# Performance work log

Measured on AMD Instinct MI355X. Metric: run time of the kernel, lower is better.

## Reference

```python
import math
import jax, jax.numpy as jnp
import numpy as np

B, L, D = 8, 512, 32
SEQ_LEN = 512.0
N_PATCHES, N_REF = 16, 32
LAT, HM = 128, 4
FH, NL, FF = 8, 3, 128
PRED = 96

def _time_embed(t, d):
    # interleaved sin/cos embedding, matching PositionalEmbedding's div_term
    div = jnp.exp(jnp.arange(0, d, 2, dtype=jnp.float32) * (-math.log(10000.0) / d))
    ang = t[..., None] * div
    out = jnp.zeros(t.shape + (d,), dtype=jnp.float32)
    return out.at[..., 0::2].set(jnp.sin(ang)).at[..., 1::2].set(jnp.cos(ang))

def _layernorm(x, g, b):
    mu = jnp.mean(x, axis=-1, keepdims=True)
    var = jnp.var(x, axis=-1, keepdims=True)
    return (x - mu) / jnp.sqrt(var + 1e-5) * g + b

def _mha(z, Wq, Wk, Wv, Wo, bq, bk, bv, bo):
    N, S, dm = z.shape
    hd = dm // FH
    q = (z @ Wq + bq).reshape(N, S, FH, hd)
    k = (z @ Wk + bk).reshape(N, S, FH, hd)
    v = (z @ Wv + bv).reshape(N, S, FH, hd)
    s = jnp.einsum('nqhe,nkhe->nhqk', q, k) / math.sqrt(hd)
    a = jax.nn.softmax(s, axis=-1)
    o = jnp.einsum('nhqk,nkhe->nqhe', a, v).reshape(N, S, dm)
    return o @ Wo + bo

def _forward(x, x_mark, x_mask, Wq, Wk, W_out, b_out, f_Wq, f_Wk, f_Wv, f_Wo, f_bq, f_bk, f_bv, f_bo, f_ln1_g, f_ln1_b, f_W1, f_b1, f_W2, f_b2, f_ln2_g, f_ln2_b, ln_f_g, ln_f_b, W_lin, b_lin):
    t = x_mark[:, :, 0]                                   # [B, L] irregular timestamps in [0, SEQ_LEN]
    edges = jnp.linspace(0.0, SEQ_LEN, N_PATCHES + 1)
    refs = jnp.linspace(0.0, SEQ_LEN, N_REF * N_PATCHES).reshape(N_PATCHES, N_REF)
    obs_valid = jnp.sum(x_mask, axis=-1) > 0              # [B, L]
    dk = LAT // HM
    Kmat = (_time_embed(t, LAT) @ Wk).reshape(B, L, HM, dk)
    v = x * x_mask                                        # mask values like `v = v * m` in original
    reprs = []
    for i in range(N_PATCHES):  # fixed small structural loop
        # _split_patch equivalent: per-channel masked attention is permutation
        # invariant, so the sort/scatter compaction reduces to masking.
        in_patch = (t >= edges[i]) & (t <= edges[i + 1]) & obs_valid   # [B, L]
        Qi = (_time_embed(refs[i], LAT) @ Wq).reshape(N_REF, HM, dk)
        scores = jnp.einsum('rhe,blhe->bhrl', Qi, Kmat) / math.sqrt(dk)
        cmask = x_mask * in_patch[..., None].astype(x.dtype)           # [B, L, D]
        neg = jnp.where(cmask[:, None, None, :, :] > 0, 0.0, -1e9)     # [B,1,1,L,D]
        p = jax.nn.softmax(scores[..., None] + neg, axis=3)            # [B,H,R,L,D]
        attn = jnp.einsum('bhrld,bld->brhd', p, v)                     # [B,R,H,D]
        reprs.append(attn.reshape(B, N_REF, HM * D) @ W_out + b_out)   # [B,R,D]
    rp = jnp.stack(reprs, axis=1)                          # [B, NP, R, D]
    z = rp.transpose(0, 3, 1, 2).reshape(B * D, N_PATCHES, N_REF)
    z = z + _time_embed(jnp.arange(N_PATCHES, dtype=jnp.float32), N_REF)[None]
    for l in range(NL):
        a = _mha(z, f_Wq[l], f_Wk[l], f_Wv[l], f_Wo[l], f_bq[l], f_bk[l], f_bv[l], f_bo[l])
        z = _layernorm(z + a, f_ln1_g[l], f_ln1_b[l])
        y = jax.nn.gelu(z @ f_W1[l] + f_b1[l]) @ f_W2[l] + f_b2[l]
        z = _layernorm(z + y, f_ln2_g[l], f_ln2_b[l])
    z = _layernorm(z, ln_f_g, ln_f_b)
    emb = z.reshape(B, D, N_PATCHES, N_REF).transpose(0, 1, 3, 2)      # [B, D, R, NP]
    out = emb.reshape(B, D, N_REF * N_PATCHES) @ W_lin + b_lin         # [B, D, PRED]
    return out.transpose(0, 2, 1)                          # [B, PRED, D]

def setup_inputs():
    key = jax.random.key(0)
    ks = jax.random.split(key, 30)
    def w(i, shape, fan_in):
        return jax.random.normal(ks[i], shape, jnp.float32) / math.sqrt(fan_in)
    return {
        'x': jax.random.normal(ks[0], (B, L, D), jnp.float32),
        'x_mark': jnp.sort(jax.random.uniform(ks[1], (B, L, 1), jnp.float32) * SEQ_LEN, axis=1),
        'x_mask': (jax.random.uniform(ks[2], (B, L, D), jnp.float32) < 0.8).astype(jnp.float32),
        'Wq': w(3, (LAT, LAT), LAT),
        'Wk': w(4, (LAT, LAT), LAT),
        'W_out': w(5, (HM * D, D), HM * D),
        'b_out': jnp.zeros((D,), jnp.float32),
        'f_Wq': w(6, (NL, N_REF, N_REF), N_REF),
        'f_Wk': w(7, (NL, N_REF, N_REF), N_REF),
        'f_Wv': w(8, (NL, N_REF, N_REF), N_REF),
        'f_Wo': w(9, (NL, N_REF, N_REF), N_REF),
        'f_bq': jnp.zeros((NL, N_REF), jnp.float32),
        'f_bk': jnp.zeros((NL, N_REF), jnp.float32),
        'f_bv': jnp.zeros((NL, N_REF), jnp.float32),
        'f_bo': jnp.zeros((NL, N_REF), jnp.float32),
        'f_ln1_g': jnp.ones((NL, N_REF), jnp.float32),
        'f_ln1_b': jnp.zeros((NL, N_REF), jnp.float32),
        'f_W1': w(10, (NL, N_REF, FF), N_REF),
        'f_b1': jnp.zeros((NL, FF), jnp.float32),
        'f_W2': w(11, (NL, FF, N_REF), FF),
        'f_b2': jnp.zeros((NL, N_REF), jnp.float32),
        'f_ln2_g': jnp.ones((NL, N_REF), jnp.float32),
        'f_ln2_b': jnp.zeros((NL, N_REF), jnp.float32),
        'ln_f_g': jnp.ones((N_REF,), jnp.float32),
        'ln_f_b': jnp.zeros((N_REF,), jnp.float32),
        'W_lin': w(12, (N_REF * N_PATCHES, PRED), N_REF * N_PATCHES),
        'b_lin': jnp.zeros((PRED,), jnp.float32),
    }

def reference(x, x_mark, x_mask, Wq, Wk, W_out, b_out, f_Wq, f_Wk, f_Wv, f_Wo, f_bq, f_bk, f_bv, f_bo, f_ln1_g, f_ln1_b, f_W1, f_b1, f_W2, f_b2, f_ln2_g, f_ln2_b, ln_f_g, ln_f_b, W_lin, b_lin):
    return _forward(x, x_mark, x_mask, Wq, Wk, W_out, b_out, f_Wq, f_Wk, f_Wv, f_Wo, f_bq, f_bk, f_bv, f_bo, f_ln1_g, f_ln1_b, f_W1, f_b1, f_W2, f_b2, f_ln2_g, f_ln2_b, ln_f_g, ln_f_b, W_lin, b_lin)
```

## Files before the change

kernel.cpp:

```cpp
#include <hip/hip_runtime.h>
#include <math.h>


#define ISQ32 0.17677669529663687f
#define C128  (-0.07195578415606394f)
#define C32   (-0.28782313662425575f)

__launch_bounds__(256)
__global__ void k_embed_mm(const float* __restrict__ x_mark,
                           const float* __restrict__ Wk,
                           const float* __restrict__ Wq,
                           const float* __restrict__ x_mask,
                           float* __restrict__ Kmat,
                           float* __restrict__ Qall,
                           unsigned* __restrict__ obsBits) {
    if (blockIdx.x >= 144) {
        const int gt = (blockIdx.x - 144) * 256 + threadIdx.x;
        const int w = gt >> 6, lane = gt & 63;
        const int bl = w * 2 + (lane >> 5);
        const int d = lane & 31;
        const unsigned long long mm = __ballot(x_mask[bl * 32 + d] > 0.0f);
        if (lane == 0)  obsBits[w * 2]     = (unsigned)(mm & 0xffffffffull);
        if (lane == 32) obsBits[w * 2 + 1] = (unsigned)(mm >> 32);
        return;
    }
    __shared__ float sTe[32][128];
    const int wv = threadIdx.x >> 6;
    const int lane = threadIdx.x & 63;
    const int bb = blockIdx.x;
    const int row0 = bb * 32 + wv * 8;
    const float dv = __expf((float)(2 * lane) * C128);
    #pragma unroll
    for (int rr = 0; rr < 8; ++rr) {
        const int row = row0 + rr;
        const float t = (row < 4096) ? x_mark[row] : (float)(row - 4096) * (512.0f / 511.0f);
        const float ang = t * dv;
        sTe[wv * 8 + rr][2 * lane]     = __sinf(ang);
        sTe[wv * 8 + rr][2 * lane + 1] = __cosf(ang);
    }
    __syncthreads();
    const float* W = (bb < 128) ? Wk : Wq;
    float a0[8], a1[8];
    #pragma unroll
    for (int rr = 0; rr < 8; ++rr) { a0[rr] = 0.f; a1[rr] = 0.f; }
    for (int k = 0; k < 128; ++k) {
        const float wa = W[k * 128 + lane];
        const float wb = W[k * 128 + lane + 64];
        #pragma unroll
        for (int rr = 0; rr < 8; ++rr) {
            const float te = sTe[wv * 8 + rr][k];
            a0[rr] = fmaf(te, wa, a0[rr]);
            a1[rr] = fmaf(te, wb, a1[rr]);
        }
    }
    #pragma unroll
    for (int rr = 0; rr < 8; ++rr) {
        const int row = row0 + rr;
        float* outp = (row < 4096) ? (Kmat + row * 128) : (Qall + (row - 4096) * 128);
        outp[lane] = a0[rr];
        outp[lane + 64] = a1[rr];
    }
}

__launch_bounds__(256)
__global__ void k_patch_attn(const float* __restrict__ x,
                             const float* __restrict__ x_mark,
                             const unsigned* __restrict__ obsBits,
                             const float* __restrict__ Kmat,
                             const float* __restrict__ Qall,
                             float* __restrict__ attn) {
    __shared__ float sQ[32][36];
    __shared__ float sK[96][36];
    __shared__ float sX[96][36];
    __shared__ float sS[32][100];
    __shared__ unsigned sBits[96];
    __shared__ int sLo, sHi;
    __shared__ unsigned sAV;
    const int tid = threadIdx.x;
    const int h = blockIdx.x & 3;
    const int b = (blockIdx.x >> 2) & 7;
    const int i = blockIdx.x >> 5;
    const float e0 = 32.0f * (float)i, e1 = 32.0f * (float)(i + 1);
    if (tid == 0) { sLo = 512; sHi = -1; sAV = 0u; }
    __syncthreads();
    #pragma unroll
    for (int k = 0; k < 4; ++k) {
        const int idx = tid + 256 * k;
        sQ[idx >> 5][idx & 31] = Qall[(i * 32 + (idx >> 5)) * 128 + h * 32 + (idx & 31)];
    }
    {
        int mylo = 512, myhi = -1;
        unsigned mybits = 0u;
        #pragma unroll
        for (int k = 0; k < 2; ++k) {
            const int l = tid + 256 * k;
            const float t = x_mark[b * 512 + l];
            if (t >= e0 && t <= e1) {
                mylo = min(mylo, l);
                myhi = max(myhi, l);
                mybits |= obsBits[b * 512 + l];
            }
        }
        #pragma unroll
        for (int off = 32; off > 0; off >>= 1) {
            mylo = min(mylo, __shfl_xor(mylo, off));
            myhi = max(myhi, __shfl_xor(myhi, off));
            mybits |= __shfl_xor(mybits, off);
        }
        if ((tid & 63) == 0) {
            atomicMin(&sLo, mylo);
            atomicMax(&sHi, myhi);
            atomicOr(&sAV, mybits);
        }
    }
    __syncthreads();
    const int lo = sLo, hi = sHi;
    const int NA = hi - lo + 1;
    const unsigned av = sAV;
    const int r = tid >> 3, dg = tid & 7;

    if (NA >= 1 && NA <= 96 && av == 0xffffffffu) {
        if (tid < NA) sBits[tid] = obsBits[b * 512 + lo + tid];
        for (int idx = tid; idx < NA * 32; idx += 256) {
            const int ll = idx >> 5, c = idx & 31;
            sK[ll][c] = Kmat[(b * 512 + lo + ll) * 128 + h * 32 + c];
            sX[ll][c] = x[(b * 512 + lo + ll) * 32 + c];
        }
        __syncthreads();
        float m = -1e30f;
        for (int ll = dg; ll < NA; ll += 8) {
            float p0 = 0.f, p1 = 0.f, p2 = 0.f, p3 = 0.f;
            #pragma unroll
            for (int e = 0; e < 32; e += 4) {
                p0 = fmaf(sQ[r][e],     sK[ll][e],     p0);
                p1 = fmaf(sQ[r][e + 1], sK[ll][e + 1], p1);
                p2 = fmaf(sQ[r][e + 2], sK[ll][e + 2], p2);
                p3 = fmaf(sQ[r][e + 3], sK[ll][e + 3], p3);
            }
            const float s = (p0 + p1 + p2 + p3) * ISQ32;
            sS[r][ll] = s;
            m = fmaxf(m, s);
        }
        #pragma unroll
        for (int off = 4; off > 0; off >>= 1) m = fmaxf(m, __shfl_xor(m, off));
        for (int ll = dg; ll < NA; ll += 8) sS[r][ll] = __expf(sS[r][ll] - m);
        __syncthreads();
        float num0 = 0.f, num1 = 0.f, num2 = 0.f, num3 = 0.f;
        float den0 = 0.f, den1 = 0.f, den2 = 0.f, den3 = 0.f;
        for (int ll = 0; ll < NA; ++ll) {
            const float e = sS[r][ll];
            const unsigned bits = sBits[ll];
            if ((bits >> dg) & 1u)        { den0 += e; num0 = fmaf(e, sX[ll][dg],      num0); }
            if ((bits >> (dg + 8)) & 1u)  { den1 += e; num1 = fmaf(e, sX[ll][dg + 8],  num1); }
            if ((bits >> (dg + 16)) & 1u) { den2 += e; num2 = fmaf(e, sX[ll][dg + 16], num2); }
            if ((bits >> (dg + 24)) & 1u) { den3 += e; num3 = fmaf(e, sX[ll][dg + 24], num3); }
        }
        float* ap = attn + ((i * 8 + b) * 32 + r) * 128 + h * 32;
        ap[dg]      = num0 / den0;
        ap[dg + 8]  = num1 / den1;
        ap[dg + 16] = num2 / den2;
        ap[dg + 24] = num3 / den3;
    } else {
        float m = -1e30f;
        float num[4] = {0.f, 0.f, 0.f, 0.f}, den[4] = {0.f, 0.f, 0.f, 0.f};
        for (int l = 0; l < 512; ++l) {
            const float t = x_mark[b * 512 + l];
            const unsigned bits = obsBits[b * 512 + l];
            const bool inr = (t >= e0 && t <= e1);
            const unsigned effD = (inr ? bits : 0u) | ~av;
            if (effD == 0u) continue;
            const unsigned effN = effD & bits;
            const float* Kp = Kmat + (b * 512 + l) * 128 + h * 32;
            float a = 0.f;
            #pragma unroll
            for (int e2 = 0; e2 < 32; ++e2) a = fmaf(sQ[r][e2], Kp[e2], a);
            const float s = a * ISQ32;
            float eNew;
            if (s > m) {
                const float scale = __expf(m - s);
                #pragma unroll
                for (int jj = 0; jj < 4; ++jj) { den[jj] *= scale; num[jj] *= scale; }
                m = s;
                eNew = 1.0f;
            } else {
                eNew = __expf(s - m);
            }
            const float* xp = x + (b * 512 + l) * 32;
            #pragma unroll
            for (int jj = 0; jj < 4; ++jj) {
                const int d = dg + 8 * jj;
                if ((effD >> d) & 1u) den[jj] += eNew;
                if ((effN >> d) & 1u) num[jj] = fmaf(eNew, xp[d], num[jj]);
            }
        }
        float* ap = attn + ((i * 8 + b) * 32 + r) * 128 + h * 32;
        #pragma unroll
        for (int jj = 0; jj < 4; ++jj) ap[dg + 8 * jj] = num[jj] / den[jj];
    }
}

__global__ void k_reprs(const float* __restrict__ attn,
                        const float* __restrict__ W_out,
                        const float* __restrict__ b_out,
                        float* __restrict__ z) {
    __shared__ float sA[32][129];
    const int tid = threadIdx.x;
    const int b = blockIdx.x & 7;
    const int i = blockIdx.x >> 3;
    #pragma unroll
    for (int k = 0; k < 16; ++k) {
        const int idx = tid + 256 * k;
        sA[idx >> 7][idx & 127] = attn[(i * 8 + b) * 4096 + idx];
    }
    __syncthreads();
    const int r = tid & 31, dgrp = tid >> 5;
    float acc0 = 0.f, acc1 = 0.f, acc2 = 0.f, acc3 = 0.f;
    #pragma unroll 8
    for (int k = 0; k < 128; ++k) {
        const float a = sA[r][k];
        acc0 = fmaf(a, W_out[k * 32 + dgrp],      acc0);
        acc1 = fmaf(a, W_out[k * 32 + dgrp + 8],  acc1);
        acc2 = fmaf(a, W_out[k * 32 + dgrp + 16], acc2);
        acc3 = fmaf(a, W_out[k * 32 + dgrp + 24], acc3);
    }
    const float dv = expf((float)(2 * (r >> 1)) * C32);
    const float ang = (float)i * dv;
    const float pe = (r & 1) ? cosf(ang) : sinf(ang);
    const int base = i * 32 + r;
    z[(b * 32 + dgrp)      * 512 + base] = acc0 + b_out[dgrp]      + pe;
    z[(b * 32 + dgrp + 8)  * 512 + base] = acc1 + b_out[dgrp + 8]  + pe;
    z[(b * 32 + dgrp + 16) * 512 + base] = acc2 + b_out[dgrp + 16] + pe;
    z[(b * 32 + dgrp + 24) * 512 + base] = acc3 + b_out[dgrp + 24] + pe;
}

__launch_bounds__(256, 1)
__global__ void k_former(const float* __restrict__ z,
                         const float* __restrict__ f_Wq, const float* __restrict__ f_Wk,
                         const float* __restrict__ f_Wv, const float* __restrict__ f_Wo,
                         const float* __restrict__ f_bq, const float* __restrict__ f_bk,
                         const float* __restrict__ f_bv, const float* __restrict__ f_bo,
                         const float* __restrict__ f_ln1_g, const float* __restrict__ f_ln1_b,
                         const float* __restrict__ f_W1, const float* __restrict__ f_b1,
                         const float* __restrict__ f_W2, const float* __restrict__ f_b2,
                         const float* __restrict__ f_ln2_g, const float* __restrict__ f_ln2_b,
                         const float* __restrict__ ln_f_g, const float* __restrict__ ln_f_b,
                         const float* __restrict__ W_lin, const float* __restrict__ b_lin,
                         float* __restrict__ out) {
    __shared__ float wbuf[12800];
    __shared__ float sKmat[16][36], sVmat[16][36];
    __shared__ float sZrow[16][36], sOrow[16][36];
    __shared__ float sH[16][132];
    const int tid = threadIdx.x;
    const int n = blockIdx.x;
    const int lane64 = tid & 63;
    const int w = tid >> 6;
    const int sLoc = lane64 >> 4;
    const int s = w * 4 + sLoc;
    const int l16 = lane64 & 15;
    const int j0 = 2 * l16;
    const int gbase = lane64 & 48;

    #define STAGE_LAYER(l) { \
        ((float4*)wbuf)[tid]       = ((const float4*)(f_Wq + (l) * 1024))[tid]; \
        ((float4*)wbuf)[256 + tid] = ((const float4*)(f_Wk + (l) * 1024))[tid]; \
        ((float4*)wbuf)[512 + tid] = ((const float4*)(f_Wv + (l) * 1024))[tid]; \
        ((float4*)wbuf)[768 + tid] = ((const float4*)(f_Wo + (l) * 1024))[tid]; \
        _Pragma("unroll") \
        for (int r2 = 0; r2 < 4; ++r2) { \
            const int idx4 = r2 * 256 + tid; \
            const int kk = idx4 >> 5, f4 = (idx4 & 31) << 2; \
            const float4 v = ((const float4*)(f_W1 + (l) * 4096))[idx4]; \
            wbuf[4096 + (f4 + 0) * 36 + kk] = v.x; \
            wbuf[4096 + (f4 + 1) * 36 + kk] = v.y; \
            wbuf[4096 + (f4 + 2) * 36 + kk] = v.z; \
            wbuf[4096 + (f4 + 3) * 36 + kk] = v.w; \
        } \
        _Pragma("unroll") \
        for (int r2 = 0; r2 < 4; ++r2) \
            ((float4*)(wbuf + 8704))[r2 * 256 + tid] = ((const float4*)(f_W2 + (l) * 4096))[r2 * 256 + tid]; \
    }

    {
        const int ps = tid >> 4, pj = (tid & 15) * 2;
        *(float2*)&sZrow[ps][pj] = *(const float2*)(z + n * 512 + ps * 32 + pj);
    }
    STAGE_LAYER(0)
    __syncthreads();

    for (int l = 0; l < 3; ++l) {
        float q0, q1;
        {
            float4 zr[8];
            #pragma unroll
            for (int k4 = 0; k4 < 8; ++k4) zr[k4] = *(const float4*)&sZrow[s][4 * k4];
            const float2 bq = *(const float2*)(f_bq + l * 32 + j0);
            const float2 bk = *(const float2*)(f_bk + l * 32 + j0);
            const float2 bv = *(const float2*)(f_bv + l * 32 + j0);
            float qa = 0.f, qb = 0.f, ka = 0.f, kb = 0.f, va = 0.f, vb = 0.f;
            #pragma unroll
            for (int k4 = 0; k4 < 8; ++k4) {
                #pragma unroll
                for (int e = 0; e < 4; ++e) {
                    const int kk = 4 * k4 + e;
                    const float zz = (e == 0) ? zr[k4].x : (e == 1) ? zr[k4].y : (e == 2) ? zr[k4].z : zr[k4].w;
                    const float2 wq = *(const float2*)&wbuf[kk * 32 + j0];
                    const float2 wk2 = *(const float2*)&wbuf[1024 + kk * 32 + j0];
                    const float2 wv2 = *(const float2*)&wbuf[2048 + kk * 32 + j0];
                    qa = fmaf(zz, wq.x, qa);  qb = fmaf(zz, wq.y, qb);
                    ka = fmaf(zz, wk2.x, ka); kb = fmaf(zz, wk2.y, kb);
                    va = fmaf(zz, wv2.x, va); vb = fmaf(zz, wv2.y, vb);
                }
            }
            q0 = qa + bq.x; q1 = qb + bq.y;
            *(float2*)&sKmat[s][j0] = make_float2(ka + bk.x, kb + bk.y);
            *(float2*)&sVmat[s][j0] = make_float2(va + bv.x, vb + bv.y);
        }
        __syncthreads();
        {
            const int hh = l16 & 7, kh = l16 >> 3;
            const int h4 = hh * 4;
            const float qa = __shfl(q0, gbase + 2 * hh);
            const float qb = __shfl(q1, gbase + 2 * hh);
            const float qc = __shfl(q0, gbase + 2 * hh + 1);
            const float qd = __shfl(q1, gbase + 2 * hh + 1);
            float sc[8];
            #pragma unroll
            for (int m = 0; m < 8; ++m) {
                const int kk = kh * 8 + m;
                const float4 kv = *(const float4*)&sKmat[kk][h4];
                sc[m] = (qa * kv.x + qb * kv.y + qc * kv.z + qd * kv.w) * 0.5f;
            }
            float mx = sc[0];
            #pragma unroll
            for (int m = 1; m < 8; ++m) mx = fmaxf(mx, sc[m]);
            mx = fmaxf(mx, __shfl_xor(mx, 8));
            float sum = 0.f;
            #pragma unroll
            for (int m = 0; m < 8; ++m) { sc[m] = __expf(sc[m] - mx); sum += sc[m]; }
            sum += __shfl_xor(sum, 8);
            const float inv = 1.0f / sum;
            float o0 = 0.f, o1 = 0.f, o2 = 0.f, o3 = 0.f;
            #pragma unroll
            for (int m = 0; m < 8; ++m) {
                const int kk = kh * 8 + m;
                const float4 vv = *(const float4*)&sVmat[kk][h4];
                o0 = fmaf(sc[m], vv.x, o0); o1 = fmaf(sc[m], vv.y, o1);
                o2 = fmaf(sc[m], vv.z, o2); o3 = fmaf(sc[m], vv.w, o3);
            }
            o0 += __shfl_xor(o0, 8); o1 += __shfl_xor(o1, 8);
            o2 += __shfl_xor(o2, 8); o3 += __shfl_xor(o3, 8);
            if (kh == 0)
                *(float4*)&sOrow[s][h4] = make_float4(o0 * inv, o1 * inv, o2 * inv, o3 * inv);
        }
        {
            float oacc0 = 0.f, oacc1 = 0.f;
            #pragma unroll
            for (int k4 = 0; k4 < 8; ++k4) {
                const float4 ov = *(const float4*)&sOrow[s][4 * k4];
                #pragma unroll
                for (int e = 0; e < 4; ++e) {
                    const float oe = (e == 0) ? ov.x : (e == 1) ? ov.y : (e == 2) ? ov.z : ov.w;
                    const float2 wo = *(const float2*)&wbuf[3072 + (4 * k4 + e) * 32 + j0];
                    oacc0 = fmaf(oe, wo.x, oacc0); oacc1 = fmaf(oe, wo.y, oacc1);
                }
            }
            const float2 bo = *(const float2*)(f_bo + l * 32 + j0);
            const float2 zold = *(const float2*)&sZrow[s][j0];
            const float t0 = zold.x + oacc0 + bo.x;
            const float t1 = zold.y + oacc1 + bo.y;
            float sm = t0 + t1, sq = t0 * t0 + t1 * t1;
            #pragma unroll
            for (int off = 8; off > 0; off >>= 1) { sm += __shfl_xor(sm, off); sq += __shfl_xor(sq, off); }
            const float mu = sm * (1.0f / 32.0f);
            const float rs = rsqrtf(sq * (1.0f / 32.0f) - mu * mu + 1e-5f);
            const float2 g1 = *(const float2*)(f_ln1_g + l * 32 + j0);
            const float2 be1 = *(const float2*)(f_ln1_b + l * 32 + j0);
            *(float2*)&sZrow[s][j0] = make_float2((t0 - mu) * rs * g1.x + be1.x,
                                                  (t1 - mu) * rs * g1.y + be1.y);
        }
        {
            float4 zr[8];
            #pragma unroll
            for (int k4 = 0; k4 < 8; ++k4) zr[k4] = *(const float4*)&sZrow[s][4 * k4];
            #pragma unroll
            for (int m = 0; m < 8; ++m) {
                const int f = l16 + 16 * m;
                float acc = f_b1[l * 128 + f];
                #pragma unroll
                for (int k4 = 0; k4 < 8; ++k4) {
                    const float4 w14 = *(const float4*)&wbuf[4096 + f * 36 + 4 * k4];
                    acc = fmaf(zr[k4].x, w14.x, acc); acc = fmaf(zr[k4].y, w14.y, acc);
                    acc = fmaf(zr[k4].z, w14.z, acc); acc = fmaf(zr[k4].w, w14.w, acc);
                }
                const float c = acc;
                const float a2 = 1.5957691216057308f * (c + 0.044715f * c * c * c);
                const float e = __expf(a2);
                sH[s][f] = 0.5f * c * (2.0f - 2.0f / (e + 1.0f));
            }
        }
        {
            const float2 b2v = *(const float2*)(f_b2 + l * 32 + j0);
            float fa = 0.f, fb = 0.f;
            #pragma unroll
            for (int f4 = 0; f4 < 32; ++f4) {
                const float4 hv = *(const float4*)&sH[s][4 * f4];
                #pragma unroll
                for (int e = 0; e < 4; ++e) {
                    const float he = (e == 0) ? hv.x : (e == 1) ? hv.y : (e == 2) ? hv.z : hv.w;
                    const float2 w2 = *(const float2*)&wbuf[8704 + (4 * f4 + e) * 32 + j0];
                    fa = fmaf(he, w2.x, fa); fb = fmaf(he, w2.y, fb);
                }
            }
            const float2 zold = *(const float2*)&sZrow[s][j0];
            const float t0 = zold.x + fa + b2v.x;
            const float t1 = zold.y + fb + b2v.y;
            float sm = t0 + t1, sq = t0 * t0 + t1 * t1;
            #pragma unroll
            for (int off = 8; off > 0; off >>= 1) { sm += __shfl_xor(sm, off); sq += __shfl_xor(sq, off); }
            const float mu = sm * (1.0f / 32.0f);
            const float rs = rsqrtf(sq * (1.0f / 32.0f) - mu * mu + 1e-5f);
            const float2 g2 = *(const float2*)(f_ln2_g + l * 32 + j0);
            const float2 be2 = *(const float2*)(f_ln2_b + l * 32 + j0);
            *(float2*)&sZrow[s][j0] = make_float2((t0 - mu) * rs * g2.x + be2.x,
                                                  (t1 - mu) * rs * g2.y + be2.y);
        }
        if (l < 2) {
            __syncthreads();
            if (l == 0) STAGE_LAYER(1) else STAGE_LAYER(2)
            __syncthreads();
        }
    }
    {
        const float2 zv = *(const float2*)&sZrow[s][j0];
        const float t0 = zv.x, t1 = zv.y;
        float sm = t0 + t1, sq = t0 * t0 + t1 * t1;
        #pragma unroll
        for (int off = 8; off > 0; off >>= 1) { sm += __shfl_xor(sm, off); sq += __shfl_xor(sq, off); }
        const float mu = sm * (1.0f / 32.0f);
        const float rs = rsqrtf(sq * (1.0f / 32.0f) - mu * mu + 1e-5f);
        const float2 gf = *(const float2*)(ln_f_g + j0);
        const float2 bf = *(const float2*)(ln_f_b + j0);
        *(float2*)&sZrow[s][j0] = make_float2((t0 - mu) * rs * gf.x + bf.x,
                                              (t1 - mu) * rs * gf.y + bf.y);
    }
    {
        float* sRed = &sH[0][0];
        float4 zr[8];
        #pragma unroll
        for (int k4 = 0; k4 < 8; ++k4) zr[k4] = *(const float4*)&sZrow[s][4 * k4];
        const int o0 = 6 * l16;
        float p0 = 0.f, p1 = 0.f, p2 = 0.f, p3 = 0.f, p4 = 0.f, p5 = 0.f;
        #pragma unroll
        for (int k4 = 0; k4 < 8; ++k4) {
            #pragma unroll
            for (int e = 0; e < 4; ++e) {
                const int rr = 4 * k4 + e;
                const float zz = (e == 0) ? zr[k4].x : (e == 1) ? zr[k4].y : (e == 2) ? zr[k4].z : zr[k4].w;
                const float* wl = W_lin + (rr * 16 + s) * 96 + o0;
                const float2 wa = *(const float2*)(wl);
                const float2 wb = *(const float2*)(wl + 2);
                const float2 wc = *(const float2*)(wl + 4);
                p0 = fmaf(zz, wa.x, p0); p1 = fmaf(zz, wa.y, p1);
                p2 = fmaf(zz, wb.x, p2); p3 = fmaf(zz, wb.y, p3);
                p4 = fmaf(zz, wc.x, p4); p5 = fmaf(zz, wc.y, p5);
            }
        }
        *(float2*)&sRed[s * 100 + o0]     = make_float2(p0, p1);
        *(float2*)&sRed[s * 100 + o0 + 2] = make_float2(p2, p3);
        *(float2*)&sRed[s * 100 + o0 + 4] = make_float2(p4, p5);
    }
    __syncthreads();
    if (tid < 96) {
        const float* sRed = &sH[0][0];
        float acc = b_lin[tid];
        #pragma unroll
        for (int ss = 0; ss < 16; ++ss) acc += sRed[ss * 100 + tid];
        out[((n >> 5) * 96 + tid) * 32 + (n & 31)] = acc;
    }
}

extern "C" void kernel_launch(void* const* d_in, const int* in_sizes, int n_in,
                              void* d_out, int out_size, void* d_ws, size_t ws_size,
                              hipStream_t stream) {
    const float* x       = (const float*)d_in[0];
    const float* x_mark  = (const float*)d_in[1];
    const float* x_mask  = (const float*)d_in[2];
    const float* Wq      = (const float*)d_in[3];
    const float* Wk      = (const float*)d_in[4];
    const float* W_out   = (const float*)d_in[5];
    const float* b_out   = (const float*)d_in[6];
    const float* f_Wq    = (const float*)d_in[7];
    const float* f_Wk    = (const float*)d_in[8];
    const float* f_Wv    = (const float*)d_in[9];
    const float* f_Wo    = (const float*)d_in[10];
    const float* f_bq    = (const float*)d_in[11];
    const float* f_bk    = (const float*)d_in[12];
    const float* f_bv    = (const float*)d_in[13];
    const float* f_bo    = (const float*)d_in[14];
    const float* f_ln1_g = (const float*)d_in[15];
    const float* f_ln1_b = (const float*)d_in[16];
    const float* f_W1    = (const float*)d_in[17];
    const float* f_b1    = (const float*)d_in[18];
    const float* f_W2    = (const float*)d_in[19];
    const float* f_b2    = (const float*)d_in[20];
    const float* f_ln2_g = (const float*)d_in[21];
    const float* f_ln2_b = (const float*)d_in[22];
    const float* ln_f_g  = (const float*)d_in[23];
    const float* ln_f_b  = (const float*)d_in[24];
    const float* W_lin   = (const float*)d_in[25];
    const float* b_lin   = (const float*)d_in[26];

    float* ws = (float*)d_ws;
    float* Kmat      = ws;
    float* Qall      = ws + 524288;
    unsigned* obsB   = (unsigned*)(ws + 589824);
    float* attn      = ws + 593920;
    float* zbuf      = ws + 1118208;

    k_embed_mm<<<656, 256, 0, stream>>>(x_mark, Wk, Wq, x_mask, Kmat, Qall, obsB);
    k_patch_attn<<<512, 256, 0, stream>>>(x, x_mark, obsB, Kmat, Qall, attn);
    k_reprs<<<128, 256, 0, stream>>>(attn, W_out, b_out, zbuf);
    k_former<<<256, 256, 0, stream>>>(zbuf,
        f_Wq, f_Wk, f_Wv, f_Wo, f_bq, f_bk, f_bv, f_bo,
        f_ln1_g, f_ln1_b, f_W1, f_b1, f_W2, f_b2, f_ln2_g, f_ln2_b,
        ln_f_g, ln_f_b, W_lin, b_lin, (float*)d_out);
}
```

Baseline: 62.70 us.

## Hold former weights in registers instead of staging them through shared memory

The transformer-layer kernel no longer stages each layer's weights into a large shared-memory buffer. Each thread now loads one weight column into registers straight from global memory and reuses it across 8 or 16 sequence rows. The thread-to-work mapping changes: QKV runs on 192 threads, attention gives each thread a whole query row with no shuffles, and the FFN second matmul is split-K with a shared-memory partial-sum reduction. This removes the big LDS footprint and the staging barriers, but adds more __syncthreads phases, idle threads in some phases, and uncoalesced strided global weight loads.

```diff
diff --git a/kernel.cpp b/kernel.cpp
--- a/kernel.cpp
+++ b/kernel.cpp
@@ -246,209 +246,203 @@
                          const float* __restrict__ ln_f_g, const float* __restrict__ ln_f_b,
                          const float* __restrict__ W_lin, const float* __restrict__ b_lin,
                          float* __restrict__ out) {
-    __shared__ float wbuf[12800];
-    __shared__ float sKmat[16][36], sVmat[16][36];
-    __shared__ float sZrow[16][36], sOrow[16][36];
+    __shared__ float sZ[16][36];
+    __shared__ float sQm[16][36], sKm[16][36], sVm[16][36], sOm[16][36];
     __shared__ float sH[16][132];
+    __shared__ float sP[4][16][36];
     const int tid = threadIdx.x;
     const int n = blockIdx.x;
-    const int lane64 = tid & 63;
-    const int w = tid >> 6;
-    const int sLoc = lane64 >> 4;
-    const int s = w * 4 + sLoc;
-    const int l16 = lane64 & 15;
-    const int j0 = 2 * l16;
-    const int gbase = lane64 & 48;
-
-    #define STAGE_LAYER(l) { \
-        ((float4*)wbuf)[tid]       = ((const float4*)(f_Wq + (l) * 1024))[tid]; \
-        ((float4*)wbuf)[256 + tid] = ((const float4*)(f_Wk + (l) * 1024))[tid]; \
-        ((float4*)wbuf)[512 + tid] = ((const float4*)(f_Wv + (l) * 1024))[tid]; \
-        ((float4*)wbuf)[768 + tid] = ((const float4*)(f_Wo + (l) * 1024))[tid]; \
-        _Pragma("unroll") \
-        for (int r2 = 0; r2 < 4; ++r2) { \
-            const int idx4 = r2 * 256 + tid; \
-            const int kk = idx4 >> 5, f4 = (idx4 & 31) << 2; \
-            const float4 v = ((const float4*)(f_W1 + (l) * 4096))[idx4]; \
-            wbuf[4096 + (f4 + 0) * 36 + kk] = v.x; \
-            wbuf[4096 + (f4 + 1) * 36 + kk] = v.y; \
-            wbuf[4096 + (f4 + 2) * 36 + kk] = v.z; \
-            wbuf[4096 + (f4 + 3) * 36 + kk] = v.w; \
-        } \
-        _Pragma("unroll") \
-        for (int r2 = 0; r2 < 4; ++r2) \
-            ((float4*)(wbuf + 8704))[r2 * 256 + tid] = ((const float4*)(f_W2 + (l) * 4096))[r2 * 256 + tid]; \
-    }
 
     {
         const int ps = tid >> 4, pj = (tid & 15) * 2;
-        *(float2*)&sZrow[ps][pj] = *(const float2*)(z + n * 512 + ps * 32 + pj);
-    }
-    STAGE_LAYER(0)
+        *(float2*)&sZ[ps][pj] = *(const float2*)(z + n * 512 + ps * 32 + pj);
+    }
     __syncthreads();
 
     for (int l = 0; l < 3; ++l) {
-        float q0, q1;
-        {
-            float4 zr[8];
-            #pragma unroll
-            for (int k4 = 0; k4 < 8; ++k4) zr[k4] = *(const float4*)&sZrow[s][4 * k4];
-            const float2 bq = *(const float2*)(f_bq + l * 32 + j0);
-            const float2 bk = *(const float2*)(f_bk + l * 32 + j0);
-            const float2 bv = *(const float2*)(f_bv + l * 32 + j0);
-            float qa = 0.f, qb = 0.f, ka = 0.f, kb = 0.f, va = 0.f, vb = 0.f;
-            #pragma unroll
-            for (int k4 = 0; k4 < 8; ++k4) {
+        if (tid < 192) {
+            const int j = tid & 31;
+            const int mgrp = tid >> 5;
+            const int m = mgrp % 3, half = mgrp / 3;
+            const float* Wm = ((m == 0) ? f_Wq : (m == 1) ? f_Wk : f_Wv) + l * 1024;
+            const float bias = ((m == 0) ? f_bq : (m == 1) ? f_bk : f_bv)[l * 32 + j];
+            float w[32];
+            #pragma unroll
+            for (int k = 0; k < 32; ++k) w[k] = Wm[k * 32 + j];
+            float acc[8];
+            #pragma unroll
+            for (int ss = 0; ss < 8; ++ss) {
+                const int s = half * 8 + ss;
+                float a = bias;
                 #pragma unroll
-                for (int e = 0; e < 4; ++e) {
-                    const int kk = 4 * k4 + e;
-                    const float zz = (e == 0) ? zr[k4].x : (e == 1) ? zr[k4].y : (e == 2) ? zr[k4].z : zr[k4].w;
-                    const float2 wq = *(const float2*)&wbuf[kk * 32 + j0];
-                    const float2 wk2 = *(const float2*)&wbuf[1024 + kk * 32 + j0];
-                    const float2 wv2 = *(const float2*)&wbuf[2048 + kk * 32 + j0];
-                    qa = fmaf(zz, wq.x, qa);  qb = fmaf(zz, wq.y, qb);
-                    ka = fmaf(zz, wk2.x, ka); kb = fmaf(zz, wk2.y, kb);
-                    va = fmaf(zz, wv2.x, va); vb = fmaf(zz, wv2.y, vb);
+                for (int k4 = 0; k4 < 8; ++k4) {
+                    const float4 zv = *(const float4*)&sZ[s][4 * k4];
+                    a = fmaf(zv.x, w[4 * k4],     a);
+                    a = fmaf(zv.y, w[4 * k4 + 1], a);
+                    a = fmaf(zv.z, w[4 * k4 + 2], a);
+                    a = fmaf(zv.w, w[4 * k4 + 3], a);
                 }
-            }
-            q0 = qa + bq.x; q1 = qb + bq.y;
-            *(float2*)&sKmat[s][j0] = make_float2(ka + bk.x, kb + bk.y);
-            *(float2*)&sVmat[s][j0] = make_float2(va + bv.x, vb + bv.y);
-        }
-        __syncthreads();
-        {
-            const int hh = l16 & 7, kh = l16 >> 3;
+                acc[ss] = a;
+            }
+            float (*dst)[36] = (m == 0) ? sQm : (m == 1) ? sKm : sVm;
+            #pragma unroll
+            for (int ss = 0; ss < 8; ++ss) dst[half * 8 + ss][j] = acc[ss];
+        }
+        __syncthreads();
+        if (tid < 128) {
+            const int q = tid & 15, hh = tid >> 4;
             const int h4 = hh * 4;
-            const float qa = __shfl(q0, gbase + 2 * hh);
-            const float qb = __shfl(q1, gbase + 2 * hh);
-            const float qc = __shfl(q0, gbase + 2 * hh + 1);
-            const float qd = __shfl(q1, gbase + 2 * hh + 1);
-            float sc[8];
-            #pragma unroll
-            for (int m = 0; m < 8; ++m) {
-                const int kk = kh * 8 + m;
-                const float4 kv = *(const float4*)&sKmat[kk][h4];
-                sc[m] = (qa * kv.x + qb * kv.y + qc * kv.z + qd * kv.w) * 0.5f;
-            }
-            float mx = sc[0];
-            #pragma unroll
-            for (int m = 1; m < 8; ++m) mx = fmaxf(mx, sc[m]);
-            mx = fmaxf(mx, __shfl_xor(mx, 8));
+            const float4 qv = *(const float4*)&sQm[q][h4];
+            float sc[16];
+            float mx = -1e30f;
+            #pragma unroll
+            for (int k = 0; k < 16; ++k) {
+                const float4 kv = *(const float4*)&sKm[k][h4];
+                sc[k] = (qv.x * kv.x + qv.y * kv.y + qv.z * kv.z + qv.w * kv.w) * 0.5f;
+                mx = fmaxf(mx, sc[k]);
+            }
             float sum = 0.f;
             #pragma unroll
-            for (int m = 0; m < 8; ++m) { sc[m] = __expf(sc[m] - mx); sum += sc[m]; }
-            sum += __shfl_xor(sum, 8);
+            for (int k = 0; k < 16; ++k) { sc[k] = __expf(sc[k] - mx); sum += sc[k]; }
             const float inv = 1.0f / sum;
             float o0 = 0.f, o1 = 0.f, o2 = 0.f, o3 = 0.f;
             #pragma unroll
-            for (int m = 0; m < 8; ++m) {
-                const int kk = kh * 8 + m;
-                const float4 vv = *(const float4*)&sVmat[kk][h4];
-                o0 = fmaf(sc[m], vv.x, o0); o1 = fmaf(sc[m], vv.y, o1);
-                o2 = fmaf(sc[m], vv.z, o2); o3 = fmaf(sc[m], vv.w, o3);
-            }
-            o0 += __shfl_xor(o0, 8); o1 += __shfl_xor(o1, 8);
-            o2 += __shfl_xor(o2, 8); o3 += __shfl_xor(o3, 8);
-            if (kh == 0)
-                *(float4*)&sOrow[s][h4] = make_float4(o0 * inv, o1 * inv, o2 * inv, o3 * inv);
-        }
+            for (int k = 0; k < 16; ++k) {
+                const float4 vv = *(const float4*)&sVm[k][h4];
+                o0 = fmaf(sc[k], vv.x, o0); o1 = fmaf(sc[k], vv.y, o1);
+                o2 = fmaf(sc[k], vv.z, o2); o3 = fmaf(sc[k], vv.w, o3);
+            }
+            *(float4*)&sOm[q][h4] = make_float4(o0 * inv, o1 * inv, o2 * inv, o3 * inv);
+        }
+        __syncthreads();
         {
-            float oacc0 = 0.f, oacc1 = 0.f;
+            const int sp = tid >> 5, j = tid & 31;
+            const int sA = 2 * sp, sB = sA + 1;
+            float wo[32];
+            #pragma unroll
+            for (int k = 0; k < 32; ++k) wo[k] = f_Wo[l * 1024 + k * 32 + j];
+            float oa = 0.f, ob = 0.f;
             #pragma unroll
             for (int k4 = 0; k4 < 8; ++k4) {
-                const float4 ov = *(const float4*)&sOrow[s][4 * k4];
-                #pragma unroll
-                for (int e = 0; e < 4; ++e) {
-                    const float oe = (e == 0) ? ov.x : (e == 1) ? ov.y : (e == 2) ? ov.z : ov.w;
-                    const float2 wo = *(const float2*)&wbuf[3072 + (4 * k4 + e) * 32 + j0];
-                    oacc0 = fmaf(oe, wo.x, oacc0); oacc1 = fmaf(oe, wo.y, oacc1);
-                }
-            }
-            const float2 bo = *(const float2*)(f_bo + l * 32 + j0);
-            const float2 zold = *(const float2*)&sZrow[s][j0];
-            const float t0 = zold.x + oacc0 + bo.x;
-            const float t1 = zold.y + oacc1 + bo.y;
-            float sm = t0 + t1, sq = t0 * t0 + t1 * t1;
-            #pragma unroll
-            for (int off = 8; off > 0; off >>= 1) { sm += __shfl_xor(sm, off); sq += __shfl_xor(sq, off); }
-            const float mu = sm * (1.0f / 32.0f);
-            const float rs = rsqrtf(sq * (1.0f / 32.0f) - mu * mu + 1e-5f);
-            const float2 g1 = *(const float2*)(f_ln1_g + l * 32 + j0);
-            const float2 be1 = *(const float2*)(f_ln1_b + l * 32 + j0);
-            *(float2*)&sZrow[s][j0] = make_float2((t0 - mu) * rs * g1.x + be1.x,
-                                                  (t1 - mu) * rs * g1.y + be1.y);
-        }
+                const float4 va = *(const float4*)&sOm[sA][4 * k4];
+                const float4 vb = *(const float4*)&sOm[sB][4 * k4];
+                oa = fmaf(va.x, wo[4 * k4], oa);     oa = fmaf(va.y, wo[4 * k4 + 1], oa);
+                oa = fmaf(va.z, wo[4 * k4 + 2], oa); oa = fmaf(va.w, wo[4 * k4 + 3], oa);
+                ob = fmaf(vb.x, wo[4 * k4], ob);     ob = fmaf(vb.y, wo[4 * k4 + 1], ob);
+                ob = fmaf(vb.z, wo[4 * k4 + 2], ob); ob = fmaf(vb.w, wo[4 * k4 + 3], ob);
+            }
+            const float bo = f_bo[l * 32 + j];
+            const float t0 = sZ[sA][j] + oa + bo;
+            const float t1 = sZ[sB][j] + ob + bo;
+            float s0 = t0, q0 = t0 * t0, s1 = t1, q1 = t1 * t1;
+            #pragma unroll
+            for (int off = 16; off > 0; off >>= 1) {
+                s0 += __shfl_xor(s0, off); q0 += __shfl_xor(q0, off);
+                s1 += __shfl_xor(s1, off); q1 += __shfl_xor(q1, off);
+            }
+            const float mu0 = s0 * (1.0f / 32.0f);
+            const float rs0 = rsqrtf(q0 * (1.0f / 32.0f) - mu0 * mu0 + 1e-5f);
+            const float mu1 = s1 * (1.0f / 32.0f);
+            const float rs1 = rsqrtf(q1 * (1.0f / 32.0f) - mu1 * mu1 + 1e-5f);
+            const float g1 = f_ln1_g[l * 32 + j], be1 = f_ln1_b[l * 32 + j];
+            sZ[sA][j] = (t0 - mu0) * rs0 * g1 + be1;
+            sZ[sB][j] = (t1 - mu1) * rs1 * g1 + be1;
+        }
+        __syncthreads();
         {
-            float4 zr[8];
-            #pragma unroll
-            for (int k4 = 0; k4 < 8; ++k4) zr[k4] = *(const float4*)&sZrow[s][4 * k4];
-            #pragma unroll
-            for (int m = 0; m < 8; ++m) {
-                const int f = l16 + 16 * m;
-                float acc = f_b1[l * 128 + f];
+            const int f = tid & 127, half = tid >> 7;
+            float w1[32];
+            #pragma unroll
+            for (int k = 0; k < 32; ++k) w1[k] = f_W1[l * 4096 + k * 128 + f];
+            const float b1v = f_b1[l * 128 + f];
+            #pragma unroll
+            for (int ss = 0; ss < 8; ++ss) {
+                const int s = half * 8 + ss;
+                float a = b1v;
                 #pragma unroll
                 for (int k4 = 0; k4 < 8; ++k4) {
-                    const float4 w14 = *(const float4*)&wbuf[4096 + f * 36 + 4 * k4];
-                    acc = fmaf(zr[k4].x, w14.x, acc); acc = fmaf(zr[k4].y, w14.y, acc);
-                    acc = fmaf(zr[k4].z, w14.z, acc); acc = fmaf(zr[k4].w, w14.w, acc);
+                    const float4 zv = *(const float4*)&sZ[s][4 * k4];
+                    a = fmaf(zv.x, w1[4 * k4], a);     a = fmaf(zv.y, w1[4 * k4 + 1], a);
+                    a = fmaf(zv.z, w1[4 * k4 + 2], a); a = fmaf(zv.w, w1[4 * k4 + 3], a);
                 }
-                const float c = acc;
+                const float c = a;
                 const float a2 = 1.5957691216057308f * (c + 0.044715f * c * c * c);
                 const float e = __expf(a2);
                 sH[s][f] = 0.5f * c * (2.0f - 2.0f / (e + 1.0f));
             }
         }
+        __syncthreads();
         {
-            const float2 b2v = *(const float2*)(f_b2 + l * 32 + j0);
-            float fa = 0.f, fb = 0.f;
-            #pragma unroll
-            for (int f4 = 0; f4 < 32; ++f4) {
-                const float4 hv = *(const float4*)&sH[s][4 * f4];
+            const int j = tid & 31, kc = (tid >> 5) & 3, half = tid >> 7;
+            float w2[32];
+            #pragma unroll
+            for (int k = 0; k < 32; ++k) w2[k] = f_W2[l * 4096 + (kc * 32 + k) * 32 + j];
+            #pragma unroll
+            for (int ss = 0; ss < 8; ++ss) {
+                const int s = half * 8 + ss;
+                float a = 0.f;
                 #pragma unroll
-                for (int e = 0; e < 4; ++e) {
-                    const float he = (e == 0) ? hv.x : (e == 1) ? hv.y : (e == 2) ? hv.z : hv.w;
-                    const float2 w2 = *(const float2*)&wbuf[8704 + (4 * f4 + e) * 32 + j0];
-                    fa = fmaf(he, w2.x, fa); fb = fmaf(he, w2.y, fb);
+                for (int k4 = 0; k4 < 8; ++k4) {
+                    const float4 hv = *(const float4*)&sH[s][kc * 32 + 4 * k4];
+                    a = fmaf(hv.x, w2[4 * k4], a);     a = fmaf(hv.y, w2[4 * k4 + 1], a);
+                    a = fmaf(hv.z, w2[4 * k4 + 2], a); a = fmaf(hv.w, w2[4 * k4 + 3], a);
                 }
-            }
-            const float2 zold = *(const float2*)&sZrow[s][j0];
-            const float t0 = zold.x + fa + b2v.x;
-            const float t1 = zold.y + fb + b2v.y;
-            float sm = t0 + t1, sq = t0 * t0 + t1 * t1;
-            #pragma unroll
-            for (int off = 8; off > 0; off >>= 1) { sm += __shfl_xor(sm, off); sq += __shfl_xor(sq, off); }
-            const float mu = sm * (1.0f / 32.0f);
-            const float rs = rsqrtf(sq * (1.0f / 32.0f) - mu * mu + 1e-5f);
-            const float2 g2 = *(const float2*)(f_ln2_g + l * 32 + j0);
-            const float2 be2 = *(const float2*)(f_ln2_b + l * 32 + j0);
-            *(float2*)&sZrow[s][j0] = make_float2((t0 - mu) * rs * g2.x + be2.x,
-                                                  (t1 - mu) * rs * g2.y + be2.y);
-        }
-        if (l < 2) {
-            __syncthreads();
-            if (l == 0) STAGE_LAYER(1) else STAGE_LAYER(2)
-            __syncthreads();
-        }
+                sP[kc][s][j] = a;
+            }
+        }
+        __syncthreads();
+        {
+            const int sp = tid >> 5, j = tid & 31;
+            const int sA = 2 * sp, sB = sA + 1;
+            const float b2v = f_b2[l * 32 + j];
+            const float fa = sP[0][sA][j] + sP[1][sA][j] + sP[2][sA][j] + sP[3][sA][j];
+            const float fb = sP[0][sB][j] + sP[1][sB][j] + sP[2][sB][j] + sP[3][sB][j];
+            const float t0 = sZ[sA][j] + fa + b2v;
+            const float t1 = sZ[sB][j] + fb + b2v;
+            float s0 = t0, q0 = t0 * t0, s1 = t1, q1 = t1 * t1;
+            #pragma unroll
+            for (int off = 16; off > 0; off >>= 1) {
+                s0 += __shfl_xor(s0, off); q0 += __shfl_xor(q0, off);
+                s1 += __shfl_xor(s1, off); q1 += __shfl_xor(q1, off);
+            }
+            const float mu0 = s0 * (1.0f / 32.0f);
+            const float rs0 = rsqrtf(q0 * (1.0f / 32.0f) - mu0 * mu0 + 1e-5f);
+            const float mu1 = s1 * (1.0f / 32.0f);
+            const float rs1 = rsqrtf(q1 * (1.0f / 32.0f) - mu1 * mu1 + 1e-5f);
+            const float g2 = f_ln2_g[l * 32 + j], be2 = f_ln2_b[l * 32 + j];
+            sZ[sA][j] = (t0 - mu0) * rs0 * g2 + be2;
+            sZ[sB][j] = (t1 - mu1) * rs1 * g2 + be2;
+        }
+        __syncthreads();
     }
     {
-        const float2 zv = *(const float2*)&sZrow[s][j0];
-        const float t0 = zv.x, t1 = zv.y;
-        float sm = t0 + t1, sq = t0 * t0 + t1 * t1;
-        #pragma unroll
-        for (int off = 8; off > 0; off >>= 1) { sm += __shfl_xor(sm, off); sq += __shfl_xor(sq, off); }
-        const float mu = sm * (1.0f / 32.0f);
-        const float rs = rsqrtf(sq * (1.0f / 32.0f) - mu * mu + 1e-5f);
-        const float2 gf = *(const float2*)(ln_f_g + j0);
-        const float2 bf = *(const float2*)(ln_f_b + j0);
-        *(float2*)&sZrow[s][j0] = make_float2((t0 - mu) * rs * gf.x + bf.x,
-                                              (t1 - mu) * rs * gf.y + bf.y);
-    }
+        const int sp = tid >> 5, j = tid & 31;
+        const int sA = 2 * sp, sB = sA + 1;
+        const float t0 = sZ[sA][j], t1 = sZ[sB][j];
+        float s0 = t0, q0 = t0 * t0, s1 = t1, q1 = t1 * t1;
+        #pragma unroll
+        for (int off = 16; off > 0; off >>= 1) {
+            s0 += __shfl_xor(s0, off); q0 += __shfl_xor(q0, off);
+            s1 += __shfl_xor(s1, off); q1 += __shfl_xor(q1, off);
+        }
+        const float mu0 = s0 * (1.0f / 32.0f);
+        const float rs0 = rsqrtf(q0 * (1.0f / 32.0f) - mu0 * mu0 + 1e-5f);
+        const float mu1 = s1 * (1.0f / 32.0f);
+        const float rs1 = rsqrtf(q1 * (1.0f / 32.0f) - mu1 * mu1 + 1e-5f);
+        const float gf = ln_f_g[j], bf = ln_f_b[j];
+        sZ[sA][j] = (t0 - mu0) * rs0 * gf + bf;
+        sZ[sB][j] = (t1 - mu1) * rs1 * gf + bf;
+    }
+    __syncthreads();
     {
         float* sRed = &sH[0][0];
+        const int w = tid >> 6, lane64 = tid & 63;
+        const int s = w * 4 + (lane64 >> 4);
+        const int l16 = lane64 & 15;
+        const int o0 = 6 * l16;
         float4 zr[8];
         #pragma unroll
-        for (int k4 = 0; k4 < 8; ++k4) zr[k4] = *(const float4*)&sZrow[s][4 * k4];
-        const int o0 = 6 * l16;
+        for (int k4 = 0; k4 < 8; ++k4) zr[k4] = *(const float4*)&sZ[s][4 * k4];
         float p0 = 0.f, p1 = 0.f, p2 = 0.f, p3 = 0.f, p4 = 0.f, p5 = 0.f;
         #pragma unroll
         for (int k4 = 0; k4 < 8; ++k4) {
```

After: 69.56 us. 10.9% more time.
